# Optimization experiments

Hardware: AMD Instinct MI355X
Metric: run time of the kernel (lower is better)

## Reference

```python
import math
import jax, jax.numpy as jnp
import numpy as np

B, S, D, H = 2, 2048, 1024, 16
DK = D // H


def setup_inputs() -> dict:
    key = jax.random.key(0)
    ks = jax.random.split(key, 11)
    s = 0.02
    return {
        "q": jax.random.normal(ks[0], (B, S, D), jnp.float32),
        "k": jax.random.normal(ks[1], (B, S, D), jnp.float32),
        "v": jax.random.normal(ks[2], (B, S, D), jnp.float32),
        # torch nn.Linear weights are [out_features, in_features]
        "w_q": jax.random.normal(ks[3], (D, D), jnp.float32) * s,
        "b_q": jax.random.normal(ks[4], (D,), jnp.float32) * s,
        "w_k": jax.random.normal(ks[5], (D, D), jnp.float32) * s,
        "b_k": jax.random.normal(ks[6], (D,), jnp.float32) * s,
        "w_v": jax.random.normal(ks[7], (D, D), jnp.float32) * s,
        "b_v": jax.random.normal(ks[8], (D,), jnp.float32) * s,
        "w_o": jax.random.normal(ks[9], (D, D), jnp.float32) * s,
        "b_o": jax.random.normal(ks[10], (D,), jnp.float32) * s,
    }


def _heads(x):
    # [B,S,D] -> [B,H,S,DK]
    return x.reshape(B, -1, H, DK).transpose(0, 2, 1, 3)


def reference(q, k, v, w_q, b_q, w_k, b_k, w_v, b_v, w_o, b_o):
    query = _heads(q @ w_q.T + b_q)
    key = _heads(k @ w_k.T + b_k)
    value = _heads(v @ w_v.T + b_v)
    # scaled scores [B,H,S,S]
    scores = jnp.einsum("bhqd,bhkd->bhqk", query, key) / math.sqrt(DK)
    # NOTE: the original torch code calls scores.softmax(dim=-1) but DISCARDS
    # the result (softmax is not in-place); faithfully, raw scaled scores are
    # used to weight the values. Dropout disabled (p=0 / eval).
    attn_out = jnp.einsum("bhqk,bhkd->bhqd", scores, value)
    x = attn_out.transpose(0, 2, 1, 3).reshape(B, -1, H * DK)
    return x @ w_o.T + b_o
```

## Files before the change

kernel.cpp:

```cpp
#include <hip/hip_runtime.h>
#include <hip/hip_bf16.h>

typedef unsigned short ushort_t;
typedef unsigned int uint32;
typedef __attribute__((ext_vector_type(8))) short short8;
typedef __attribute__((ext_vector_type(4))) float f32x4;

#define NB 2
#define NS 2048
#define ND 1024
#define NH 16

__device__ __forceinline__ float bf2f(ushort_t u) {
  return __uint_as_float(((uint32)u) << 16);
}
__device__ __forceinline__ ushort_t f2bf(float x) {
  uint32 u = __float_as_uint(x);
  uint32 r = u + 0x7FFFu + ((u >> 16) & 1u);
  return (ushort_t)(r >> 16);
}

__device__ __forceinline__ void gload16(const void* g, void* l) {
  __builtin_amdgcn_global_load_lds(
      (const __attribute__((address_space(1))) void*)g,
      (__attribute__((address_space(3))) void*)l, 16, 0, 0);
}

__global__ __launch_bounds__(256) void convert_kernel(
    const float* q, const float* k, const float* v, const float* wq,
    const float* wk, const float* wv, const float* wo, ushort_t* Xq,
    ushort_t* Xk, ushort_t* Xv, ushort_t* Wq, ushort_t* Wk, ushort_t* Wv,
    ushort_t* Wo) {
  const int blk = blockIdx.x;
  const float* src;
  ushort_t* dst;
  int base;
  if (blk < 2048) { src = q; dst = Xq; base = blk; }
  else if (blk < 4096) { src = k; dst = Xk; base = blk - 2048; }
  else if (blk < 6144) { src = v; dst = Xv; base = blk - 4096; }
  else if (blk < 6656) { src = wq; dst = Wq; base = blk - 6144; }
  else if (blk < 7168) { src = wk; dst = Wk; base = blk - 6656; }
  else if (blk < 7680) { src = wv; dst = Wv; base = blk - 7168; }
  else { src = wo; dst = Wo; base = blk - 7680; }
  const size_t off = (size_t)base * 2048 + (size_t)threadIdx.x * 8;
  const float4 v0 = *(const float4*)&src[off];
  const float4 v1 = *(const float4*)&src[off + 4];
  short8 o;
  o[0] = (short)f2bf(v0.x); o[1] = (short)f2bf(v0.y);
  o[2] = (short)f2bf(v0.z); o[3] = (short)f2bf(v0.w);
  o[4] = (short)f2bf(v1.x); o[5] = (short)f2bf(v1.y);
  o[6] = (short)f2bf(v1.z); o[7] = (short)f2bf(v1.w);
  *(short8*)&dst[off] = o;
}

template <typename OutT>
__device__ __forceinline__ void gemm128x128(
    const ushort_t* __restrict__ A, const ushort_t* __restrict__ Bt,
    const float* __restrict__ bias, OutT* __restrict__ Y, int bm, int bn) {
  constexpr int K = 1024;
  constexpr int NY = 1024;
  __shared__ __align__(16) ushort_t sA[128 * 32];
  __shared__ __align__(16) ushort_t sB[128 * 32];
  const int t = threadIdx.x;
  const int lane = t & 63;
  const int w = t >> 6;
  const int wr = w >> 1, wc = w & 1;
  const int r15 = lane & 15, kh = lane >> 4;
  const int m0 = bm * 128, n0 = bn * 128;

  f32x4 acc[4][4] = {};

  const int row0 = t >> 2, cc8 = (t & 3) * 8;
  const ushort_t* gA0 = A + (size_t)(m0 + row0) * K + cc8;
  const ushort_t* gA1 = A + (size_t)(m0 + row0 + 64) * K + cc8;
  const ushort_t* gB0 = Bt + (size_t)(n0 + row0) * K + cc8;
  const ushort_t* gB1 = Bt + (size_t)(n0 + row0 + 64) * K + cc8;
  ushort_t* lA0 = &sA[t * 8];
  ushort_t* lA1 = &sA[(t + 256) * 8];
  ushort_t* lB0 = &sB[t * 8];
  ushort_t* lB1 = &sB[(t + 256) * 8];

  for (int k0 = 0; k0 < K; k0 += 32) {
    gload16(gA0 + k0, lA0);
    gload16(gA1 + k0, lA1);
    gload16(gB0 + k0, lB0);
    gload16(gB1 + k0, lB1);
    __syncthreads();
    short8 af[4], bfr[4];
#pragma unroll
    for (int m = 0; m < 4; ++m)
      af[m] = *(const short8*)&sA[(wr * 64 + m * 16 + r15) * 32 + kh * 8];
#pragma unroll
    for (int n = 0; n < 4; ++n)
      bfr[n] = *(const short8*)&sB[(wc * 64 + n * 16 + r15) * 32 + kh * 8];
#pragma unroll
    for (int m = 0; m < 4; ++m)
#pragma unroll
      for (int n = 0; n < 4; ++n)
        acc[m][n] = __builtin_amdgcn_mfma_f32_16x16x32_bf16(af[m], bfr[n],
                                                            acc[m][n], 0, 0, 0);
    __syncthreads();
  }

  const int orow0 = m0 + wr * 64 + kh * 4;
  const int ocol0 = n0 + wc * 64 + r15;
#pragma unroll
  for (int m = 0; m < 4; ++m) {
#pragma unroll
    for (int n = 0; n < 4; ++n) {
      const int col = ocol0 + n * 16;
      const float bv = bias[col];
#pragma unroll
      for (int j = 0; j < 4; ++j) {
        const int row = orow0 + m * 16 + j;
        const float val = acc[m][n][j] + bv;
        if constexpr (__is_same(OutT, ushort_t))
          Y[(size_t)row * NY + col] = f2bf(val);
        else
          Y[(size_t)row * NY + col] = val;
      }
    }
  }
}

template <typename OutT>
__device__ __forceinline__ void gemm64x128(
    const ushort_t* __restrict__ A, const ushort_t* __restrict__ Bt,
    const float* __restrict__ bias, OutT* __restrict__ Y, int bm, int bn) {
  constexpr int K = 1024;
  constexpr int NY = 1024;
  __shared__ __align__(16) ushort_t sA[64 * 32];
  __shared__ __align__(16) ushort_t sB[128 * 32];
  const int t = threadIdx.x;
  const int lane = t & 63;
  const int w = t >> 6;
  const int wr = w >> 1, wc = w & 1;
  const int r15 = lane & 15, kh = lane >> 4;
  const int m0 = bm * 64, n0 = bn * 128;

  f32x4 acc[2][4] = {};

  const int rowA = t >> 2, cc8 = (t & 3) * 8;
  const ushort_t* gA = A + (size_t)(m0 + rowA) * K + cc8;
  const ushort_t* gB0 = Bt + (size_t)(n0 + rowA) * K + cc8;
  const ushort_t* gB1 = Bt + (size_t)(n0 + rowA + 64) * K + cc8;
  ushort_t* lA = &sA[t * 8];
  ushort_t* lB0 = &sB[t * 8];
  ushort_t* lB1 = &sB[(t + 256) * 8];

  for (int k0 = 0; k0 < K; k0 += 32) {
    gload16(gA + k0, lA);
    gload16(gB0 + k0, lB0);
    gload16(gB1 + k0, lB1);
    __syncthreads();
    short8 af[2], bfr[4];
#pragma unroll
    for (int m = 0; m < 2; ++m)
      af[m] = *(const short8*)&sA[(wr * 32 + m * 16 + r15) * 32 + kh * 8];
#pragma unroll
    for (int n = 0; n < 4; ++n)
      bfr[n] = *(const short8*)&sB[(wc * 64 + n * 16 + r15) * 32 + kh * 8];
#pragma unroll
    for (int m = 0; m < 2; ++m)
#pragma unroll
      for (int n = 0; n < 4; ++n)
        acc[m][n] = __builtin_amdgcn_mfma_f32_16x16x32_bf16(af[m], bfr[n],
                                                            acc[m][n], 0, 0, 0);
    __syncthreads();
  }

  const int orow0 = m0 + wr * 32 + kh * 4;
  const int ocol0 = n0 + wc * 64 + r15;
#pragma unroll
  for (int m = 0; m < 2; ++m) {
#pragma unroll
    for (int n = 0; n < 4; ++n) {
      const int col = ocol0 + n * 16;
      const float bv = bias[col];
#pragma unroll
      for (int j = 0; j < 4; ++j) {
        const int row = orow0 + m * 16 + j;
        const float val = acc[m][n][j] + bv;
        if constexpr (__is_same(OutT, ushort_t))
          Y[(size_t)row * NY + col] = f2bf(val);
        else
          Y[(size_t)row * NY + col] = val;
      }
    }
  }
}

__global__ __launch_bounds__(256) void proj_qkv_kernel(
    const ushort_t* Xq, const ushort_t* Xk, const ushort_t* Xv,
    const ushort_t* Wq, const ushort_t* Wk, const ushort_t* Wv,
    const float* bq, const float* bk, const float* bv,
    ushort_t* Qb, ushort_t* Kb, ushort_t* Vb) {
  const int blk = blockIdx.x;
  const int tsel = blk >> 8;
  int rem = blk & 255;
  rem = (rem & 7) * 32 + (rem >> 3);
  const int bm = rem >> 3, bn = rem & 7;
  const ushort_t* A = tsel == 0 ? Xq : (tsel == 1 ? Xk : Xv);
  const ushort_t* Bt = tsel == 0 ? Wq : (tsel == 1 ? Wk : Wv);
  const float* bias = tsel == 0 ? bq : (tsel == 1 ? bk : bv);
  ushort_t* Y = tsel == 0 ? Qb : (tsel == 1 ? Kb : Vb);
  gemm128x128<ushort_t>(A, Bt, bias, Y, bm, bn);
}

__global__ __launch_bounds__(256) void out_gemm_kernel(
    const ushort_t* Qb, const ushort_t* Ct, const float* bo, float* out) {
  int blk = blockIdx.x;
  blk = (blk & 7) * 64 + (blk >> 3);
  const int bm = blk >> 3, bn = blk & 7;
  const ushort_t* Bt = Ct + (size_t)(bm >> 5) * 1024 * 1024;
  gemm64x128<float>(Qb, Bt, bo, out, bm, bn);
}

__global__ __launch_bounds__(256) void kv_outer_kernel(
    const ushort_t* __restrict__ Kb, const ushort_t* __restrict__ Vb,
    float* __restrict__ Mpart) {
  const int bh = blockIdx.x >> 4;
  const int c = blockIdx.x & 15;
  const int b = bh >> 4, h = bh & 15;
  __shared__ __align__(16) ushort_t sK[128][64];
  __shared__ __align__(16) ushort_t sV[128][64];
  const int t = threadIdx.x;
  const ushort_t* baseK = Kb + (size_t)(b * NS + c * 128) * ND + h * 64;
  const ushort_t* baseV = Vb + (size_t)(b * NS + c * 128) * ND + h * 64;
#pragma unroll
  for (int i = 0; i < 4; ++i) {
    const int ch = t + i * 256;
    const int row = ch >> 3, cc = ch & 7;
    *(short8*)&sK[row][cc * 8] = *(const short8*)&baseK[(size_t)row * ND + cc * 8];
    *(short8*)&sV[row][cc * 8] = *(const short8*)&baseV[(size_t)row * ND + cc * 8];
  }
  __syncthreads();
  const int d1 = (t & 15) * 4, d2 = (t >> 4) * 4;
  float acc[4][4] = {};
  for (int s = 0; s < 128; ++s) {
    const uint2 ku = *(const uint2*)&sK[s][d1];
    const uint2 vu = *(const uint2*)&sV[s][d2];
    float kx[4], vx[4];
    kx[0] = __uint_as_float(ku.x << 16);
    kx[1] = __uint_as_float(ku.x & 0xFFFF0000u);
    kx[2] = __uint_as_float(ku.y << 16);
    kx[3] = __uint_as_float(ku.y & 0xFFFF0000u);
    vx[0] = __uint_as_float(vu.x << 16);
    vx[1] = __uint_as_float(vu.x & 0xFFFF0000u);
    vx[2] = __uint_as_float(vu.y << 16);
    vx[3] = __uint_as_float(vu.y & 0xFFFF0000u);
#pragma unroll
    for (int a2 = 0; a2 < 4; ++a2)
#pragma unroll
      for (int b2 = 0; b2 < 4; ++b2) acc[a2][b2] += kx[a2] * vx[b2];
  }
  float* outp = Mpart + ((size_t)bh * 16 + c) * 4096;
#pragma unroll
  for (int a2 = 0; a2 < 4; ++a2)
#pragma unroll
    for (int b2 = 0; b2 < 4; ++b2)
      outp[(d1 + a2) * 64 + (d2 + b2)] = acc[a2][b2];
}

__global__ __launch_bounds__(256) void reduce_M_kernel(
    const float* __restrict__ Mpart, float* __restrict__ Mred) {
  const int idx = blockIdx.x * 256 + threadIdx.x;
  const int bh = idx >> 12, e = idx & 4095;
  float s = 0.f;
#pragma unroll
  for (int c = 0; c < 16; ++c) s += Mpart[((size_t)bh * 16 + c) * 4096 + e];
  Mred[idx] = s * 0.125f;
}

__global__ __launch_bounds__(256) void build_C_kernel(
    const float* __restrict__ Mred, const ushort_t* __restrict__ Wo,
    ushort_t* __restrict__ Ct) {
  const int blk = blockIdx.x;
  const int b = blk >> 8, h = (blk >> 4) & 15, jb = blk & 15;
  __shared__ float sM[64][65];
  __shared__ __align__(16) ushort_t sW[64][72];
  const int t = threadIdx.x;
  const float* Mp = Mred + (size_t)(b * 16 + h) * 4096;
#pragma unroll
  for (int i = 0; i < 16; ++i) {
    const int e = t + i * 256;
    sM[e >> 6][e & 63] = Mp[e];
  }
  const int j0 = jb * 64;
#pragma unroll
  for (int i = 0; i < 2; ++i) {
    const int ch = t + i * 256;
    const int row = ch >> 3, cc = ch & 7;
    *(short8*)&sW[row][cc * 8] =
        *(const short8*)&Wo[(size_t)(j0 + row) * ND + h * 64 + cc * 8];
  }
  __syncthreads();
  const int kk = (t & 15) * 4, jj = (t >> 4) * 4;
  float acc[4][4] = {};
  for (int i = 0; i < 64; ++i) {
    float mv[4], wv[4];
#pragma unroll
    for (int a2 = 0; a2 < 4; ++a2) mv[a2] = sM[kk + a2][i];
#pragma unroll
    for (int b2 = 0; b2 < 4; ++b2) wv[b2] = bf2f(sW[jj + b2][i]);
#pragma unroll
    for (int a2 = 0; a2 < 4; ++a2)
#pragma unroll
      for (int b2 = 0; b2 < 4; ++b2) acc[a2][b2] += mv[a2] * wv[b2];
  }
#pragma unroll
  for (int a2 = 0; a2 < 4; ++a2)
#pragma unroll
    for (int b2 = 0; b2 < 4; ++b2)
      Ct[((size_t)b * ND + j0 + jj + b2) * ND + h * 64 + kk + a2] =
          f2bf(acc[a2][b2]);
}

extern "C" void kernel_launch(void* const* d_in, const int* in_sizes, int n_in,
                              void* d_out, int out_size, void* d_ws,
                              size_t ws_size, hipStream_t stream) {
  (void)in_sizes; (void)n_in; (void)out_size; (void)ws_size;
  const float* q = (const float*)d_in[0];
  const float* k = (const float*)d_in[1];
  const float* v = (const float*)d_in[2];
  const float* wq = (const float*)d_in[3];
  const float* bq = (const float*)d_in[4];
  const float* wk = (const float*)d_in[5];
  const float* bk = (const float*)d_in[6];
  const float* wv = (const float*)d_in[7];
  const float* bv = (const float*)d_in[8];
  const float* wo = (const float*)d_in[9];
  const float* bo = (const float*)d_in[10];
  float* out = (float*)d_out;

  const size_t MB = 1048576;
  char* ws = (char*)d_ws;
  ushort_t* Xq = (ushort_t*)(ws + 0 * MB);
  ushort_t* Xk = (ushort_t*)(ws + 8 * MB);
  ushort_t* Xv = (ushort_t*)(ws + 16 * MB);
  ushort_t* Wq = (ushort_t*)(ws + 24 * MB);
  ushort_t* Wk = (ushort_t*)(ws + 26 * MB);
  ushort_t* Wv = (ushort_t*)(ws + 28 * MB);
  ushort_t* Wo = (ushort_t*)(ws + 30 * MB);
  ushort_t* Qb = (ushort_t*)(ws + 32 * MB);
  ushort_t* Kb = (ushort_t*)(ws + 40 * MB);
  ushort_t* Vb = (ushort_t*)(ws + 48 * MB);
  float* Mpart = (float*)(ws + 0 * MB);
  float* Mred = (float*)(ws + 8 * MB);
  ushort_t* Ct = (ushort_t*)(ws + 8 * MB + 524288);

  hipLaunchKernelGGL(convert_kernel, dim3(8192), dim3(256), 0, stream, q, k, v,
                     wq, wk, wv, wo, Xq, Xk, Xv, Wq, Wk, Wv, Wo);
  hipLaunchKernelGGL(proj_qkv_kernel, dim3(768), dim3(256), 0, stream, Xq, Xk,
                     Xv, Wq, Wk, Wv, bq, bk, bv, Qb, Kb, Vb);
  hipLaunchKernelGGL(kv_outer_kernel, dim3(512), dim3(256), 0, stream, Kb, Vb,
                     Mpart);
  hipLaunchKernelGGL(reduce_M_kernel, dim3(512), dim3(256), 0, stream, Mpart,
                     Mred);
  hipLaunchKernelGGL(build_C_kernel, dim3(512), dim3(256), 0, stream, Mred, Wo,
                     Ct);
  hipLaunchKernelGGL(out_gemm_kernel, dim3(512), dim3(256), 0, stream, Qb, Ct,
                     bo, out);
}
```

Before: 205.9 us.

## Fuse fp32-to-bf16 activation conversion into QKV GEMM and double-buffer GEMMs

Removes the separate conversion pass over the q/k/v activations. The QKV projection GEMM now loads fp32 A tiles into registers, converts them to bf16 and writes them to LDS itself, so the bf16 activation copies are no longer written to and read back from global memory. Both the projection GEMM and the output GEMM gain double-buffered LDS with prefetch of the next tile, which lets loads overlap MFMA work. The cost is doubled LDS per block, more registers, and fp32 activation reads: each A tile is re-read by all 8 column blocks at twice the byte size.

```diff
diff --git a/kernel.cpp b/kernel.cpp
--- a/kernel.cpp
+++ b/kernel.cpp
@@ -4,6 +4,7 @@
 typedef unsigned short ushort_t;
 typedef unsigned int uint32;
 typedef __attribute__((ext_vector_type(8))) short short8;
+typedef __attribute__((ext_vector_type(4))) short short4_t;
 typedef __attribute__((ext_vector_type(4))) float f32x4;
 
 #define NB 2
@@ -26,22 +27,17 @@
       (__attribute__((address_space(3))) void*)l, 16, 0, 0);
 }
 
-__global__ __launch_bounds__(256) void convert_kernel(
-    const float* q, const float* k, const float* v, const float* wq,
-    const float* wk, const float* wv, const float* wo, ushort_t* Xq,
-    ushort_t* Xk, ushort_t* Xv, ushort_t* Wq, ushort_t* Wk, ushort_t* Wv,
-    ushort_t* Wo) {
+__global__ __launch_bounds__(256) void convert_w_kernel(
+    const float* wq, const float* wk, const float* wv, const float* wo,
+    ushort_t* Wq, ushort_t* Wk, ushort_t* Wv, ushort_t* Wo) {
   const int blk = blockIdx.x;
   const float* src;
   ushort_t* dst;
   int base;
-  if (blk < 2048) { src = q; dst = Xq; base = blk; }
-  else if (blk < 4096) { src = k; dst = Xk; base = blk - 2048; }
-  else if (blk < 6144) { src = v; dst = Xv; base = blk - 4096; }
-  else if (blk < 6656) { src = wq; dst = Wq; base = blk - 6144; }
-  else if (blk < 7168) { src = wk; dst = Wk; base = blk - 6656; }
-  else if (blk < 7680) { src = wv; dst = Wv; base = blk - 7168; }
-  else { src = wo; dst = Wo; base = blk - 7680; }
+  if (blk < 512) { src = wq; dst = Wq; base = blk; }
+  else if (blk < 1024) { src = wk; dst = Wk; base = blk - 512; }
+  else if (blk < 1536) { src = wv; dst = Wv; base = blk - 1024; }
+  else { src = wo; dst = Wo; base = blk - 1536; }
   const size_t off = (size_t)base * 2048 + (size_t)threadIdx.x * 8;
   const float4 v0 = *(const float4*)&src[off];
   const float4 v1 = *(const float4*)&src[off + 4];
@@ -53,14 +49,14 @@
   *(short8*)&dst[off] = o;
 }
 
-template <typename OutT>
-__device__ __forceinline__ void gemm128x128(
-    const ushort_t* __restrict__ A, const ushort_t* __restrict__ Bt,
-    const float* __restrict__ bias, OutT* __restrict__ Y, int bm, int bn) {
+__device__ __forceinline__ void gemm128x128_f32A(
+    const float* __restrict__ A, const ushort_t* __restrict__ Bt,
+    const float* __restrict__ bias, ushort_t* __restrict__ Y, int bm, int bn) {
   constexpr int K = 1024;
+  constexpr int NT = K / 32;
   constexpr int NY = 1024;
-  __shared__ __align__(16) ushort_t sA[128 * 32];
-  __shared__ __align__(16) ushort_t sB[128 * 32];
+  __shared__ __align__(16) ushort_t sA[2 * 128 * 32];
+  __shared__ __align__(16) ushort_t sB[2 * 128 * 32];
   const int t = threadIdx.x;
   const int lane = t & 63;
   const int w = t >> 6;
@@ -70,29 +66,60 @@
 
   f32x4 acc[4][4] = {};
 
-  const int row0 = t >> 2, cc8 = (t & 3) * 8;
-  const ushort_t* gA0 = A + (size_t)(m0 + row0) * K + cc8;
-  const ushort_t* gA1 = A + (size_t)(m0 + row0 + 64) * K + cc8;
-  const ushort_t* gB0 = Bt + (size_t)(n0 + row0) * K + cc8;
-  const ushort_t* gB1 = Bt + (size_t)(n0 + row0 + 64) * K + cc8;
-  ushort_t* lA0 = &sA[t * 8];
-  ushort_t* lA1 = &sA[(t + 256) * 8];
-  ushort_t* lB0 = &sB[t * 8];
-  ushort_t* lB1 = &sB[(t + 256) * 8];
-
-  for (int k0 = 0; k0 < K; k0 += 32) {
-    gload16(gA0 + k0, lA0);
-    gload16(gA1 + k0, lA1);
-    gload16(gB0 + k0, lB0);
-    gload16(gB1 + k0, lB1);
-    __syncthreads();
+  const int rowA = t >> 3, c4 = t & 7;
+  const float* gA = A + (size_t)(m0 + rowA) * K + c4 * 4;
+  const int rowB = t >> 2, cc8 = (t & 3) * 8;
+  const ushort_t* gB0 = Bt + (size_t)(n0 + rowB) * K + cc8;
+  const ushort_t* gB1 = Bt + (size_t)(n0 + rowB + 64) * K + cc8;
+
+  float4 ar[4];
+#define LOADA(tile)                                                        \
+  {                                                                        \
+    const int k0_ = (tile) * 32;                                           \
+    _Pragma("unroll") for (int i = 0; i < 4; ++i) ar[i] =                  \
+        *(const float4*)&gA[(size_t)(i * 32) * K + k0_];                   \
+  }
+#define WRITEA(bufsel)                                                     \
+  {                                                                        \
+    ushort_t* sAw_ = &sA[(bufsel) * 4096];                                 \
+    _Pragma("unroll") for (int i = 0; i < 4; ++i) {                        \
+      short4_t s_;                                                         \
+      s_[0] = (short)f2bf(ar[i].x);                                        \
+      s_[1] = (short)f2bf(ar[i].y);                                        \
+      s_[2] = (short)f2bf(ar[i].z);                                        \
+      s_[3] = (short)f2bf(ar[i].w);                                        \
+      *(short4_t*)&sAw_[(rowA + i * 32) * 32 + c4 * 4] = s_;               \
+    }                                                                      \
+  }
+#define STAGEB(tile, bufsel)                                               \
+  {                                                                        \
+    ushort_t* sBw_ = &sB[(bufsel) * 4096];                                 \
+    gload16(gB0 + (tile) * 32, &sBw_[t * 8]);                              \
+    gload16(gB1 + (tile) * 32, &sBw_[(t + 256) * 8]);                      \
+  }
+
+  LOADA(0);
+  STAGEB(0, 0);
+  WRITEA(0);
+  LOADA(1);
+  __syncthreads();
+
+  int cur = 0;
+  for (int tt = 0; tt < NT; ++tt) {
+    if (tt + 1 < NT) {
+      WRITEA(cur ^ 1);
+      STAGEB(tt + 1, cur ^ 1);
+      if (tt + 2 < NT) LOADA(tt + 2);
+    }
+    const ushort_t* sAc = &sA[cur * 4096];
+    const ushort_t* sBc = &sB[cur * 4096];
     short8 af[4], bfr[4];
 #pragma unroll
     for (int m = 0; m < 4; ++m)
-      af[m] = *(const short8*)&sA[(wr * 64 + m * 16 + r15) * 32 + kh * 8];
+      af[m] = *(const short8*)&sAc[(wr * 64 + m * 16 + r15) * 32 + kh * 8];
 #pragma unroll
     for (int n = 0; n < 4; ++n)
-      bfr[n] = *(const short8*)&sB[(wc * 64 + n * 16 + r15) * 32 + kh * 8];
+      bfr[n] = *(const short8*)&sBc[(wc * 64 + n * 16 + r15) * 32 + kh * 8];
 #pragma unroll
     for (int m = 0; m < 4; ++m)
 #pragma unroll
@@ -100,7 +127,11 @@
         acc[m][n] = __builtin_amdgcn_mfma_f32_16x16x32_bf16(af[m], bfr[n],
                                                             acc[m][n], 0, 0, 0);
     __syncthreads();
-  }
+    cur ^= 1;
+  }
+#undef LOADA
+#undef WRITEA
+#undef STAGEB
 
   const int orow0 = m0 + wr * 64 + kh * 4;
   const int ocol0 = n0 + wc * 64 + r15;
@@ -113,24 +144,20 @@
 #pragma unroll
       for (int j = 0; j < 4; ++j) {
         const int row = orow0 + m * 16 + j;
-        const float val = acc[m][n][j] + bv;
-        if constexpr (__is_same(OutT, ushort_t))
-          Y[(size_t)row * NY + col] = f2bf(val);
-        else
-          Y[(size_t)row * NY + col] = val;
+        Y[(size_t)row * NY + col] = f2bf(acc[m][n][j] + bv);
       }
     }
   }
 }
 
-template <typename OutT>
-__device__ __forceinline__ void gemm64x128(
+__device__ __forceinline__ void gemm64x128_dbuf(
     const ushort_t* __restrict__ A, const ushort_t* __restrict__ Bt,
-    const float* __restrict__ bias, OutT* __restrict__ Y, int bm, int bn) {
+    const float* __restrict__ bias, float* __restrict__ Y, int bm, int bn) {
   constexpr int K = 1024;
+  constexpr int NT = K / 32;
   constexpr int NY = 1024;
-  __shared__ __align__(16) ushort_t sA[64 * 32];
-  __shared__ __align__(16) ushort_t sB[128 * 32];
+  __shared__ __align__(16) ushort_t sA[2 * 64 * 32];
+  __shared__ __align__(16) ushort_t sB[2 * 128 * 32];
   const int t = threadIdx.x;
   const int lane = t & 63;
   const int w = t >> 6;
@@ -140,26 +167,34 @@
 
   f32x4 acc[2][4] = {};
 
-  const int rowA = t >> 2, cc8 = (t & 3) * 8;
-  const ushort_t* gA = A + (size_t)(m0 + rowA) * K + cc8;
-  const ushort_t* gB0 = Bt + (size_t)(n0 + rowA) * K + cc8;
-  const ushort_t* gB1 = Bt + (size_t)(n0 + rowA + 64) * K + cc8;
-  ushort_t* lA = &sA[t * 8];
-  ushort_t* lB0 = &sB[t * 8];
-  ushort_t* lB1 = &sB[(t + 256) * 8];
-
-  for (int k0 = 0; k0 < K; k0 += 32) {
-    gload16(gA + k0, lA);
-    gload16(gB0 + k0, lB0);
-    gload16(gB1 + k0, lB1);
-    __syncthreads();
+  const int rowX = t >> 2, cc8 = (t & 3) * 8;
+  const ushort_t* gA = A + (size_t)(m0 + rowX) * K + cc8;
+  const ushort_t* gB0 = Bt + (size_t)(n0 + rowX) * K + cc8;
+  const ushort_t* gB1 = Bt + (size_t)(n0 + rowX + 64) * K + cc8;
+
+#define STAGE(tile, bufsel)                                                \
+  {                                                                        \
+    const int k0_ = (tile) * 32;                                           \
+    gload16(gA + k0_, &sA[(bufsel) * 2048 + t * 8]);                       \
+    gload16(gB0 + k0_, &sB[(bufsel) * 4096 + t * 8]);                      \
+    gload16(gB1 + k0_, &sB[(bufsel) * 4096 + (t + 256) * 8]);              \
+  }
+
+  STAGE(0, 0);
+  __syncthreads();
+
+  int cur = 0;
+  for (int tt = 0; tt < NT; ++tt) {
+    if (tt + 1 < NT) STAGE(tt + 1, cur ^ 1);
+    const ushort_t* sAc = &sA[cur * 2048];
+    const ushort_t* sBc = &sB[cur * 4096];
     short8 af[2], bfr[4];
 #pragma unroll
     for (int m = 0; m < 2; ++m)
-      af[m] = *(const short8*)&sA[(wr * 32 + m * 16 + r15) * 32 + kh * 8];
+      af[m] = *(const short8*)&sAc[(wr * 32 + m * 16 + r15) * 32 + kh * 8];
 #pragma unroll
     for (int n = 0; n < 4; ++n)
-      bfr[n] = *(const short8*)&sB[(wc * 64 + n * 16 + r15) * 32 + kh * 8];
+      bfr[n] = *(const short8*)&sBc[(wc * 64 + n * 16 + r15) * 32 + kh * 8];
 #pragma unroll
     for (int m = 0; m < 2; ++m)
 #pragma unroll
@@ -167,7 +202,9 @@
         acc[m][n] = __builtin_amdgcn_mfma_f32_16x16x32_bf16(af[m], bfr[n],
                                                             acc[m][n], 0, 0, 0);
     __syncthreads();
-  }
+    cur ^= 1;
+  }
+#undef STAGE
 
   const int orow0 = m0 + wr * 32 + kh * 4;
   const int ocol0 = n0 + wc * 64 + r15;
@@ -180,18 +217,14 @@
 #pragma unroll
       for (int j = 0; j < 4; ++j) {
         const int row = orow0 + m * 16 + j;
-        const float val = acc[m][n][j] + bv;
-        if constexpr (__is_same(OutT, ushort_t))
-          Y[(size_t)row * NY + col] = f2bf(val);
-        else
-          Y[(size_t)row * NY + col] = val;
+        Y[(size_t)row * NY + col] = acc[m][n][j] + bv;
       }
     }
   }
 }
 
 __global__ __launch_bounds__(256) void proj_qkv_kernel(
-    const ushort_t* Xq, const ushort_t* Xk, const ushort_t* Xv,
+    const float* q, const float* k, const float* v,
     const ushort_t* Wq, const ushort_t* Wk, const ushort_t* Wv,
     const float* bq, const float* bk, const float* bv,
     ushort_t* Qb, ushort_t* Kb, ushort_t* Vb) {
@@ -200,11 +233,11 @@
   int rem = blk & 255;
   rem = (rem & 7) * 32 + (rem >> 3);
   const int bm = rem >> 3, bn = rem & 7;
-  const ushort_t* A = tsel == 0 ? Xq : (tsel == 1 ? Xk : Xv);
+  const float* A = tsel == 0 ? q : (tsel == 1 ? k : v);
   const ushort_t* Bt = tsel == 0 ? Wq : (tsel == 1 ? Wk : Wv);
   const float* bias = tsel == 0 ? bq : (tsel == 1 ? bk : bv);
   ushort_t* Y = tsel == 0 ? Qb : (tsel == 1 ? Kb : Vb);
-  gemm128x128<ushort_t>(A, Bt, bias, Y, bm, bn);
+  gemm128x128_f32A(A, Bt, bias, Y, bm, bn);
 }
 
 __global__ __launch_bounds__(256) void out_gemm_kernel(
@@ -213,7 +246,7 @@
   blk = (blk & 7) * 64 + (blk >> 3);
   const int bm = blk >> 3, bn = blk & 7;
   const ushort_t* Bt = Ct + (size_t)(bm >> 5) * 1024 * 1024;
-  gemm64x128<float>(Qb, Bt, bo, out, bm, bn);
+  gemm64x128_dbuf(Qb, Bt, bo, out, bm, bn);
 }
 
 __global__ __launch_bounds__(256) void kv_outer_kernel(
@@ -335,24 +368,21 @@
 
   const size_t MB = 1048576;
   char* ws = (char*)d_ws;
-  ushort_t* Xq = (ushort_t*)(ws + 0 * MB);
-  ushort_t* Xk = (ushort_t*)(ws + 8 * MB);
-  ushort_t* Xv = (ushort_t*)(ws + 16 * MB);
-  ushort_t* Wq = (ushort_t*)(ws + 24 * MB);
-  ushort_t* Wk = (ushort_t*)(ws + 26 * MB);
-  ushort_t* Wv = (ushort_t*)(ws + 28 * MB);
-  ushort_t* Wo = (ushort_t*)(ws + 30 * MB);
-  ushort_t* Qb = (ushort_t*)(ws + 32 * MB);
-  ushort_t* Kb = (ushort_t*)(ws + 40 * MB);
-  ushort_t* Vb = (ushort_t*)(ws + 48 * MB);
-  float* Mpart = (float*)(ws + 0 * MB);
-  float* Mred = (float*)(ws + 8 * MB);
-  ushort_t* Ct = (ushort_t*)(ws + 8 * MB + 524288);
-
-  hipLaunchKernelGGL(convert_kernel, dim3(8192), dim3(256), 0, stream, q, k, v,
-                     wq, wk, wv, wo, Xq, Xk, Xv, Wq, Wk, Wv, Wo);
-  hipLaunchKernelGGL(proj_qkv_kernel, dim3(768), dim3(256), 0, stream, Xq, Xk,
-                     Xv, Wq, Wk, Wv, bq, bk, bv, Qb, Kb, Vb);
+  ushort_t* Wq = (ushort_t*)(ws + 0 * MB);
+  ushort_t* Wk = (ushort_t*)(ws + 2 * MB);
+  ushort_t* Wv = (ushort_t*)(ws + 4 * MB);
+  ushort_t* Wo = (ushort_t*)(ws + 6 * MB);
+  ushort_t* Qb = (ushort_t*)(ws + 8 * MB);
+  ushort_t* Kb = (ushort_t*)(ws + 16 * MB);
+  ushort_t* Vb = (ushort_t*)(ws + 24 * MB);
+  float* Mpart = (float*)(ws + 32 * MB);
+  float* Mred = (float*)(ws + 40 * MB);
+  ushort_t* Ct = (ushort_t*)(ws + 40 * MB + 524288);
+
+  hipLaunchKernelGGL(convert_w_kernel, dim3(2048), dim3(256), 0, stream, wq, wk,
+                     wv, wo, Wq, Wk, Wv, Wo);
+  hipLaunchKernelGGL(proj_qkv_kernel, dim3(768), dim3(256), 0, stream, q, k, v,
+                     Wq, Wk, Wv, bq, bk, bv, Qb, Kb, Vb);
   hipLaunchKernelGGL(kv_outer_kernel, dim3(512), dim3(256), 0, stream, Kb, Vb,
                      Mpart);
   hipLaunchKernelGGL(reduce_M_kernel, dim3(512), dim3(256), 0, stream, Mpart,
```

New measurement: 209.9 us. No clear change (+2.0%).

## Fold Q projection into the output matrix to skip the Q GEMM

Applied to the files above, without the earlier changes.

Instead of projecting Q (a 4096x1024x1024 GEMM) and then multiplying by the per-batch combined matrix Ct, this precomputes E = Ct·Wq per batch (a smaller 1024^3 GEMM per batch) plus a folded bias Ct·bq+bo. The final GEMM then consumes the converted raw q directly. It adds a transpose kernel for Wq, a small GEMV kernel for the bias and an extra GEMM launch. The extra bf16 rounding of E is a precision risk, and the 16-block bias kernel may serialize.

```diff
diff --git a/kernel.cpp b/kernel.cpp
--- a/kernel.cpp
+++ b/kernel.cpp
@@ -27,10 +27,9 @@
 }
 
 __global__ __launch_bounds__(256) void convert_kernel(
-    const float* q, const float* k, const float* v, const float* wq,
-    const float* wk, const float* wv, const float* wo, ushort_t* Xq,
-    ushort_t* Xk, ushort_t* Xv, ushort_t* Wq, ushort_t* Wk, ushort_t* Wv,
-    ushort_t* Wo) {
+    const float* q, const float* k, const float* v, const float* wk,
+    const float* wv, const float* wo, ushort_t* Xq, ushort_t* Xk, ushort_t* Xv,
+    ushort_t* Wk, ushort_t* Wv, ushort_t* Wo) {
   const int blk = blockIdx.x;
   const float* src;
   ushort_t* dst;
@@ -38,10 +37,9 @@
   if (blk < 2048) { src = q; dst = Xq; base = blk; }
   else if (blk < 4096) { src = k; dst = Xk; base = blk - 2048; }
   else if (blk < 6144) { src = v; dst = Xv; base = blk - 4096; }
-  else if (blk < 6656) { src = wq; dst = Wq; base = blk - 6144; }
-  else if (blk < 7168) { src = wk; dst = Wk; base = blk - 6656; }
-  else if (blk < 7680) { src = wv; dst = Wv; base = blk - 7168; }
-  else { src = wo; dst = Wo; base = blk - 7680; }
+  else if (blk < 6656) { src = wk; dst = Wk; base = blk - 6144; }
+  else if (blk < 7168) { src = wv; dst = Wv; base = blk - 6656; }
+  else { src = wo; dst = Wo; base = blk - 7168; }
   const size_t off = (size_t)base * 2048 + (size_t)threadIdx.x * 8;
   const float4 v0 = *(const float4*)&src[off];
   const float4 v1 = *(const float4*)&src[off + 4];
@@ -51,6 +49,36 @@
   o[4] = (short)f2bf(v1.x); o[5] = (short)f2bf(v1.y);
   o[6] = (short)f2bf(v1.z); o[7] = (short)f2bf(v1.w);
   *(short8*)&dst[off] = o;
+}
+
+__global__ __launch_bounds__(256) void transp_wq_kernel(const float* wq,
+                                                        ushort_t* WqT) {
+  const int tk = blockIdx.x >> 4, td = blockIdx.x & 15;
+  __shared__ float sT[64][65];
+  const int t = threadIdx.x;
+  const int r = t >> 2;
+  const int cbase = (t & 3) * 16;
+  const float* src = wq + (size_t)(tk * 64 + r) * ND + td * 64 + cbase;
+#pragma unroll
+  for (int i = 0; i < 4; ++i) {
+    const float4 v4 = *(const float4*)&src[i * 4];
+    sT[cbase + i * 4 + 0][r] = v4.x;
+    sT[cbase + i * 4 + 1][r] = v4.y;
+    sT[cbase + i * 4 + 2][r] = v4.z;
+    sT[cbase + i * 4 + 3][r] = v4.w;
+  }
+  __syncthreads();
+  const int dl = t >> 2;
+  const int kc = (t & 3) * 16;
+  ushort_t* dst = WqT + (size_t)(td * 64 + dl) * ND + tk * 64 + kc;
+  short8 o0, o1;
+#pragma unroll
+  for (int e = 0; e < 8; ++e) {
+    o0[e] = (short)f2bf(sT[dl][kc + e]);
+    o1[e] = (short)f2bf(sT[dl][kc + 8 + e]);
+  }
+  *(short8*)&dst[0] = o0;
+  *(short8*)&dst[8] = o1;
 }
 
 template <typename OutT>
@@ -109,7 +137,7 @@
 #pragma unroll
     for (int n = 0; n < 4; ++n) {
       const int col = ocol0 + n * 16;
-      const float bv = bias[col];
+      const float bv = bias ? bias[col] : 0.0f;
 #pragma unroll
       for (int j = 0; j < 4; ++j) {
         const int row = orow0 + m * 16 + j;
@@ -176,7 +204,7 @@
 #pragma unroll
     for (int n = 0; n < 4; ++n) {
       const int col = ocol0 + n * 16;
-      const float bv = bias[col];
+      const float bv = bias ? bias[col] : 0.0f;
 #pragma unroll
       for (int j = 0; j < 4; ++j) {
         const int row = orow0 + m * 16 + j;
@@ -190,30 +218,45 @@
   }
 }
 
-__global__ __launch_bounds__(256) void proj_qkv_kernel(
-    const ushort_t* Xq, const ushort_t* Xk, const ushort_t* Xv,
-    const ushort_t* Wq, const ushort_t* Wk, const ushort_t* Wv,
-    const float* bq, const float* bk, const float* bv,
-    ushort_t* Qb, ushort_t* Kb, ushort_t* Vb) {
+__global__ __launch_bounds__(256) void proj_kv_kernel(
+    const ushort_t* Xk, const ushort_t* Xv, const ushort_t* Wk,
+    const ushort_t* Wv, const float* bk, const float* bv, ushort_t* Kb,
+    ushort_t* Vb) {
   const int blk = blockIdx.x;
   const int tsel = blk >> 8;
   int rem = blk & 255;
   rem = (rem & 7) * 32 + (rem >> 3);
   const int bm = rem >> 3, bn = rem & 7;
-  const ushort_t* A = tsel == 0 ? Xq : (tsel == 1 ? Xk : Xv);
-  const ushort_t* Bt = tsel == 0 ? Wq : (tsel == 1 ? Wk : Wv);
-  const float* bias = tsel == 0 ? bq : (tsel == 1 ? bk : bv);
-  ushort_t* Y = tsel == 0 ? Qb : (tsel == 1 ? Kb : Vb);
+  const ushort_t* A = tsel == 0 ? Xk : Xv;
+  const ushort_t* Bt = tsel == 0 ? Wk : Wv;
+  const float* bias = tsel == 0 ? bk : bv;
+  ushort_t* Y = tsel == 0 ? Kb : Vb;
   gemm128x128<ushort_t>(A, Bt, bias, Y, bm, bn);
 }
 
-__global__ __launch_bounds__(256) void out_gemm_kernel(
-    const ushort_t* Qb, const ushort_t* Ct, const float* bo, float* out) {
+__global__ __launch_bounds__(256) void e_gemm_kernel(const ushort_t* Ct,
+                                                     const ushort_t* WqT,
+                                                     ushort_t* E) {
+  int blk = blockIdx.x;
+  blk = (blk & 7) * 32 + (blk >> 3);
+  const int b = blk >> 7;
+  const int rem = blk & 127;
+  const int bm = rem >> 3, bn = rem & 7;
+  const ushort_t* A = Ct + (size_t)b * ND * ND;
+  ushort_t* Y = E + (size_t)b * ND * ND;
+  gemm64x128<ushort_t>(A, WqT, nullptr, Y, bm, bn);
+}
+
+__global__ __launch_bounds__(256) void out_gemm_kernel(const ushort_t* Xq,
+                                                       const ushort_t* E,
+                                                       const float* fbias,
+                                                       float* out) {
   int blk = blockIdx.x;
   blk = (blk & 7) * 64 + (blk >> 3);
   const int bm = blk >> 3, bn = blk & 7;
-  const ushort_t* Bt = Ct + (size_t)(bm >> 5) * 1024 * 1024;
-  gemm64x128<float>(Qb, Bt, bo, out, bm, bn);
+  const int batch = bm >> 5;
+  const ushort_t* Bt = E + (size_t)batch * ND * ND;
+  gemm64x128<float>(Xq, Bt, fbias + batch * ND, out, bm, bn);
 }
 
 __global__ __launch_bounds__(256) void kv_outer_kernel(
@@ -314,6 +357,27 @@
     for (int b2 = 0; b2 < 4; ++b2)
       Ct[((size_t)b * ND + j0 + jj + b2) * ND + h * 64 + kk + a2] =
           f2bf(acc[a2][b2]);
+}
+
+__global__ __launch_bounds__(256) void f_kernel(const ushort_t* __restrict__ Ct,
+                                                const float* __restrict__ bq,
+                                                const float* __restrict__ bo,
+                                                float* __restrict__ fbias) {
+  const int b = blockIdx.x >> 3;
+  const int j = (blockIdx.x & 7) * 128 + (threadIdx.x >> 1);
+  const int half = threadIdx.x & 1;
+  const ushort_t* row = Ct + ((size_t)b * ND + j) * ND + half * 512;
+  const float* bqh = bq + half * 512;
+  float s = 0.f;
+  for (int c = 0; c < 64; ++c) {
+    const short8 v8 = *(const short8*)&row[c * 8];
+#pragma unroll
+    for (int e = 0; e < 8; ++e) s += bf2f((ushort_t)v8[e]) * bqh[c * 8 + e];
+  }
+  __shared__ float red[256];
+  red[threadIdx.x] = s;
+  __syncthreads();
+  if (half == 0) fbias[b * ND + j] = red[threadIdx.x] + red[threadIdx.x + 1] + bo[j];
 }
 
 extern "C" void kernel_launch(void* const* d_in, const int* in_sizes, int n_in,
@@ -338,27 +402,34 @@
   ushort_t* Xq = (ushort_t*)(ws + 0 * MB);
   ushort_t* Xk = (ushort_t*)(ws + 8 * MB);
   ushort_t* Xv = (ushort_t*)(ws + 16 * MB);
-  ushort_t* Wq = (ushort_t*)(ws + 24 * MB);
-  ushort_t* Wk = (ushort_t*)(ws + 26 * MB);
-  ushort_t* Wv = (ushort_t*)(ws + 28 * MB);
-  ushort_t* Wo = (ushort_t*)(ws + 30 * MB);
-  ushort_t* Qb = (ushort_t*)(ws + 32 * MB);
-  ushort_t* Kb = (ushort_t*)(ws + 40 * MB);
-  ushort_t* Vb = (ushort_t*)(ws + 48 * MB);
-  float* Mpart = (float*)(ws + 0 * MB);
-  float* Mred = (float*)(ws + 8 * MB);
-  ushort_t* Ct = (ushort_t*)(ws + 8 * MB + 524288);
-
-  hipLaunchKernelGGL(convert_kernel, dim3(8192), dim3(256), 0, stream, q, k, v,
-                     wq, wk, wv, wo, Xq, Xk, Xv, Wq, Wk, Wv, Wo);
-  hipLaunchKernelGGL(proj_qkv_kernel, dim3(768), dim3(256), 0, stream, Xq, Xk,
-                     Xv, Wq, Wk, Wv, bq, bk, bv, Qb, Kb, Vb);
+  ushort_t* Wk = (ushort_t*)(ws + 24 * MB);
+  ushort_t* Wv = (ushort_t*)(ws + 26 * MB);
+  ushort_t* Wo = (ushort_t*)(ws + 28 * MB);
+  ushort_t* WqT = (ushort_t*)(ws + 30 * MB);
+  ushort_t* Kb = (ushort_t*)(ws + 32 * MB);
+  ushort_t* Vb = (ushort_t*)(ws + 40 * MB);
+  float* Mpart = (float*)(ws + 8 * MB);
+  float* Mred = (float*)(ws + 16 * MB);
+  ushort_t* Ct = (ushort_t*)(ws + 16 * MB + 524288);
+  float* fbias = (float*)(ws + 16 * MB + 524288 + 4 * MB);
+  ushort_t* E = (ushort_t*)(ws + 24 * MB);
+
+  hipLaunchKernelGGL(convert_kernel, dim3(7680), dim3(256), 0, stream, q, k, v,
+                     wk, wv, wo, Xq, Xk, Xv, Wk, Wv, Wo);
+  hipLaunchKernelGGL(transp_wq_kernel, dim3(256), dim3(256), 0, stream, wq,
+                     WqT);
+  hipLaunchKernelGGL(proj_kv_kernel, dim3(512), dim3(256), 0, stream, Xk, Xv,
+                     Wk, Wv, bk, bv, Kb, Vb);
   hipLaunchKernelGGL(kv_outer_kernel, dim3(512), dim3(256), 0, stream, Kb, Vb,
                      Mpart);
   hipLaunchKernelGGL(reduce_M_kernel, dim3(512), dim3(256), 0, stream, Mpart,
                      Mred);
   hipLaunchKernelGGL(build_C_kernel, dim3(512), dim3(256), 0, stream, Mred, Wo,
                      Ct);
-  hipLaunchKernelGGL(out_gemm_kernel, dim3(512), dim3(256), 0, stream, Qb, Ct,
-                     bo, out);
-}
+  hipLaunchKernelGGL(f_kernel, dim3(16), dim3(256), 0, stream, Ct, bq, bo,
+                     fbias);
+  hipLaunchKernelGGL(e_gemm_kernel, dim3(256), dim3(256), 0, stream, Ct, WqT,
+                     E);
+  hipLaunchKernelGGL(out_gemm_kernel, dim3(512), dim3(256), 0, stream, Xq, E,
+                     fbias, out);
+}
```

Result: slower. 229.1 us (+11.3%).

## Use BK=64 XOR-swizzled GEMM tiles and fold M reduction into atomics

Applied to the files above, without the earlier changes.

Both bf16 GEMMs now stage 64-wide K slices per iteration, using an XOR-swizzled LDS layout to avoid bank conflicts. This halves the number of barrier pairs per K loop. The separate reduce kernel is removed: partial KᵀV outer products are atomically added into a buffer zeroed by extra convert blocks, and the 1/8 scale moves into build_C. This saves one launch and the partial-buffer traffic, at the cost of float atomic contention and non-deterministic summation order.

```diff
diff --git a/kernel.cpp b/kernel.cpp
--- a/kernel.cpp
+++ b/kernel.cpp
@@ -30,8 +30,15 @@
     const float* q, const float* k, const float* v, const float* wq,
     const float* wk, const float* wv, const float* wo, ushort_t* Xq,
     ushort_t* Xk, ushort_t* Xv, ushort_t* Wq, ushort_t* Wk, ushort_t* Wv,
-    ushort_t* Wo) {
+    ushort_t* Wo, float* Mred) {
   const int blk = blockIdx.x;
+  if (blk >= 8192) {
+    const size_t o = (size_t)(blk - 8192) * 2048 + (size_t)threadIdx.x * 8;
+    const float4 z = make_float4(0.f, 0.f, 0.f, 0.f);
+    *(float4*)&Mred[o] = z;
+    *(float4*)&Mred[o + 4] = z;
+    return;
+  }
   const float* src;
   ushort_t* dst;
   int base;
@@ -54,13 +61,13 @@
 }
 
 template <typename OutT>
-__device__ __forceinline__ void gemm128x128(
+__device__ __forceinline__ void gemm128x128_bk64(
     const ushort_t* __restrict__ A, const ushort_t* __restrict__ Bt,
     const float* __restrict__ bias, OutT* __restrict__ Y, int bm, int bn) {
   constexpr int K = 1024;
   constexpr int NY = 1024;
-  __shared__ __align__(16) ushort_t sA[128 * 32];
-  __shared__ __align__(16) ushort_t sB[128 * 32];
+  __shared__ __align__(16) ushort_t sA[128 * 64];
+  __shared__ __align__(16) ushort_t sB[128 * 64];
   const int t = threadIdx.x;
   const int lane = t & 63;
   const int w = t >> 6;
@@ -70,35 +77,39 @@
 
   f32x4 acc[4][4] = {};
 
-  const int row0 = t >> 2, cc8 = (t & 3) * 8;
-  const ushort_t* gA0 = A + (size_t)(m0 + row0) * K + cc8;
-  const ushort_t* gA1 = A + (size_t)(m0 + row0 + 64) * K + cc8;
-  const ushort_t* gB0 = Bt + (size_t)(n0 + row0) * K + cc8;
-  const ushort_t* gB1 = Bt + (size_t)(n0 + row0 + 64) * K + cc8;
-  ushort_t* lA0 = &sA[t * 8];
-  ushort_t* lA1 = &sA[(t + 256) * 8];
-  ushort_t* lB0 = &sB[t * 8];
-  ushort_t* lB1 = &sB[(t + 256) * 8];
-
-  for (int k0 = 0; k0 < K; k0 += 32) {
-    gload16(gA0 + k0, lA0);
-    gload16(gA1 + k0, lA1);
-    gload16(gB0 + k0, lB0);
-    gload16(gB1 + k0, lB1);
+  const int rowS = t >> 3;
+  const int srcSlot = (t & 7) ^ (rowS & 7);
+  const ushort_t* gA = A + (size_t)(m0 + rowS) * K + srcSlot * 8;
+  const ushort_t* gB = Bt + (size_t)(n0 + rowS) * K + srcSlot * 8;
+
+  for (int k0 = 0; k0 < K; k0 += 64) {
+#pragma unroll
+    for (int i = 0; i < 4; ++i) {
+      gload16(gA + (size_t)(i * 32) * K + k0, &sA[(t + i * 256) * 8]);
+      gload16(gB + (size_t)(i * 32) * K + k0, &sB[(t + i * 256) * 8]);
+    }
     __syncthreads();
-    short8 af[4], bfr[4];
-#pragma unroll
-    for (int m = 0; m < 4; ++m)
-      af[m] = *(const short8*)&sA[(wr * 64 + m * 16 + r15) * 32 + kh * 8];
-#pragma unroll
-    for (int n = 0; n < 4; ++n)
-      bfr[n] = *(const short8*)&sB[(wc * 64 + n * 16 + r15) * 32 + kh * 8];
-#pragma unroll
-    for (int m = 0; m < 4; ++m)
-#pragma unroll
-      for (int n = 0; n < 4; ++n)
-        acc[m][n] = __builtin_amdgcn_mfma_f32_16x16x32_bf16(af[m], bfr[n],
-                                                            acc[m][n], 0, 0, 0);
+#pragma unroll
+    for (int kk = 0; kk < 2; ++kk) {
+      const int slotbase = kk * 4 + kh;
+      short8 af[4], bfr[4];
+#pragma unroll
+      for (int m = 0; m < 4; ++m) {
+        const int row = wr * 64 + m * 16 + r15;
+        af[m] = *(const short8*)&sA[row * 64 + ((slotbase ^ (row & 7)) * 8)];
+      }
+#pragma unroll
+      for (int n = 0; n < 4; ++n) {
+        const int row = wc * 64 + n * 16 + r15;
+        bfr[n] = *(const short8*)&sB[row * 64 + ((slotbase ^ (row & 7)) * 8)];
+      }
+#pragma unroll
+      for (int m = 0; m < 4; ++m)
+#pragma unroll
+        for (int n = 0; n < 4; ++n)
+          acc[m][n] = __builtin_amdgcn_mfma_f32_16x16x32_bf16(
+              af[m], bfr[n], acc[m][n], 0, 0, 0);
+    }
     __syncthreads();
   }
 
@@ -124,13 +135,13 @@
 }
 
 template <typename OutT>
-__device__ __forceinline__ void gemm64x128(
+__device__ __forceinline__ void gemm64x128_bk64(
     const ushort_t* __restrict__ A, const ushort_t* __restrict__ Bt,
     const float* __restrict__ bias, OutT* __restrict__ Y, int bm, int bn) {
   constexpr int K = 1024;
   constexpr int NY = 1024;
-  __shared__ __align__(16) ushort_t sA[64 * 32];
-  __shared__ __align__(16) ushort_t sB[128 * 32];
+  __shared__ __align__(16) ushort_t sA[64 * 64];
+  __shared__ __align__(16) ushort_t sB[128 * 64];
   const int t = threadIdx.x;
   const int lane = t & 63;
   const int w = t >> 6;
@@ -140,32 +151,40 @@
 
   f32x4 acc[2][4] = {};
 
-  const int rowA = t >> 2, cc8 = (t & 3) * 8;
-  const ushort_t* gA = A + (size_t)(m0 + rowA) * K + cc8;
-  const ushort_t* gB0 = Bt + (size_t)(n0 + rowA) * K + cc8;
-  const ushort_t* gB1 = Bt + (size_t)(n0 + rowA + 64) * K + cc8;
-  ushort_t* lA = &sA[t * 8];
-  ushort_t* lB0 = &sB[t * 8];
-  ushort_t* lB1 = &sB[(t + 256) * 8];
-
-  for (int k0 = 0; k0 < K; k0 += 32) {
-    gload16(gA + k0, lA);
-    gload16(gB0 + k0, lB0);
-    gload16(gB1 + k0, lB1);
+  const int rowS = t >> 3;
+  const int srcSlot = (t & 7) ^ (rowS & 7);
+  const ushort_t* gA = A + (size_t)(m0 + rowS) * K + srcSlot * 8;
+  const ushort_t* gB = Bt + (size_t)(n0 + rowS) * K + srcSlot * 8;
+
+  for (int k0 = 0; k0 < K; k0 += 64) {
+#pragma unroll
+    for (int i = 0; i < 2; ++i)
+      gload16(gA + (size_t)(i * 32) * K + k0, &sA[(t + i * 256) * 8]);
+#pragma unroll
+    for (int i = 0; i < 4; ++i)
+      gload16(gB + (size_t)(i * 32) * K + k0, &sB[(t + i * 256) * 8]);
     __syncthreads();
-    short8 af[2], bfr[4];
-#pragma unroll
-    for (int m = 0; m < 2; ++m)
-      af[m] = *(const short8*)&sA[(wr * 32 + m * 16 + r15) * 32 + kh * 8];
-#pragma unroll
-    for (int n = 0; n < 4; ++n)
-      bfr[n] = *(const short8*)&sB[(wc * 64 + n * 16 + r15) * 32 + kh * 8];
-#pragma unroll
-    for (int m = 0; m < 2; ++m)
-#pragma unroll
-      for (int n = 0; n < 4; ++n)
-        acc[m][n] = __builtin_amdgcn_mfma_f32_16x16x32_bf16(af[m], bfr[n],
-                                                            acc[m][n], 0, 0, 0);
+#pragma unroll
+    for (int kk = 0; kk < 2; ++kk) {
+      const int slotbase = kk * 4 + kh;
+      short8 af[2], bfr[4];
+#pragma unroll
+      for (int m = 0; m < 2; ++m) {
+        const int row = wr * 32 + m * 16 + r15;
+        af[m] = *(const short8*)&sA[row * 64 + ((slotbase ^ (row & 7)) * 8)];
+      }
+#pragma unroll
+      for (int n = 0; n < 4; ++n) {
+        const int row = wc * 64 + n * 16 + r15;
+        bfr[n] = *(const short8*)&sB[row * 64 + ((slotbase ^ (row & 7)) * 8)];
+      }
+#pragma unroll
+      for (int m = 0; m < 2; ++m)
+#pragma unroll
+        for (int n = 0; n < 4; ++n)
+          acc[m][n] = __builtin_amdgcn_mfma_f32_16x16x32_bf16(
+              af[m], bfr[n], acc[m][n], 0, 0, 0);
+    }
     __syncthreads();
   }
 
@@ -204,7 +223,7 @@
   const ushort_t* Bt = tsel == 0 ? Wq : (tsel == 1 ? Wk : Wv);
   const float* bias = tsel == 0 ? bq : (tsel == 1 ? bk : bv);
   ushort_t* Y = tsel == 0 ? Qb : (tsel == 1 ? Kb : Vb);
-  gemm128x128<ushort_t>(A, Bt, bias, Y, bm, bn);
+  gemm128x128_bk64<ushort_t>(A, Bt, bias, Y, bm, bn);
 }
 
 __global__ __launch_bounds__(256) void out_gemm_kernel(
@@ -213,12 +232,12 @@
   blk = (blk & 7) * 64 + (blk >> 3);
   const int bm = blk >> 3, bn = blk & 7;
   const ushort_t* Bt = Ct + (size_t)(bm >> 5) * 1024 * 1024;
-  gemm64x128<float>(Qb, Bt, bo, out, bm, bn);
+  gemm64x128_bk64<float>(Qb, Bt, bo, out, bm, bn);
 }
 
 __global__ __launch_bounds__(256) void kv_outer_kernel(
     const ushort_t* __restrict__ Kb, const ushort_t* __restrict__ Vb,
-    float* __restrict__ Mpart) {
+    float* __restrict__ Mred) {
   const int bh = blockIdx.x >> 4;
   const int c = blockIdx.x & 15;
   const int b = bh >> 4, h = bh & 15;
@@ -254,22 +273,12 @@
 #pragma unroll
       for (int b2 = 0; b2 < 4; ++b2) acc[a2][b2] += kx[a2] * vx[b2];
   }
-  float* outp = Mpart + ((size_t)bh * 16 + c) * 4096;
+  float* outp = Mred + (size_t)bh * 4096;
 #pragma unroll
   for (int a2 = 0; a2 < 4; ++a2)
 #pragma unroll
     for (int b2 = 0; b2 < 4; ++b2)
-      outp[(d1 + a2) * 64 + (d2 + b2)] = acc[a2][b2];
-}
-
-__global__ __launch_bounds__(256) void reduce_M_kernel(
-    const float* __restrict__ Mpart, float* __restrict__ Mred) {
-  const int idx = blockIdx.x * 256 + threadIdx.x;
-  const int bh = idx >> 12, e = idx & 4095;
-  float s = 0.f;
-#pragma unroll
-  for (int c = 0; c < 16; ++c) s += Mpart[((size_t)bh * 16 + c) * 4096 + e];
-  Mred[idx] = s * 0.125f;
+      atomicAdd(&outp[(d1 + a2) * 64 + (d2 + b2)], acc[a2][b2]);
 }
 
 __global__ __launch_bounds__(256) void build_C_kernel(
@@ -313,7 +322,7 @@
 #pragma unroll
     for (int b2 = 0; b2 < 4; ++b2)
       Ct[((size_t)b * ND + j0 + jj + b2) * ND + h * 64 + kk + a2] =
-          f2bf(acc[a2][b2]);
+          f2bf(acc[a2][b2] * 0.125f);
 }
 
 extern "C" void kernel_launch(void* const* d_in, const int* in_sizes, int n_in,
@@ -345,17 +354,14 @@
   ushort_t* Qb = (ushort_t*)(ws + 32 * MB);
   ushort_t* Kb = (ushort_t*)(ws + 40 * MB);
   ushort_t* Vb = (ushort_t*)(ws + 48 * MB);
-  float* Mpart = (float*)(ws + 0 * MB);
-  float* Mred = (float*)(ws + 8 * MB);
-  ushort_t* Ct = (ushort_t*)(ws + 8 * MB + 524288);
-
-  hipLaunchKernelGGL(convert_kernel, dim3(8192), dim3(256), 0, stream, q, k, v,
-                     wq, wk, wv, wo, Xq, Xk, Xv, Wq, Wk, Wv, Wo);
+  float* Mred = (float*)(ws + 56 * MB);
+  ushort_t* Ct = (ushort_t*)(ws + 57 * MB);
+
+  hipLaunchKernelGGL(convert_kernel, dim3(8256), dim3(256), 0, stream, q, k, v,
+                     wq, wk, wv, wo, Xq, Xk, Xv, Wq, Wk, Wv, Wo, Mred);
   hipLaunchKernelGGL(proj_qkv_kernel, dim3(768), dim3(256), 0, stream, Xq, Xk,
                      Xv, Wq, Wk, Wv, bq, bk, bv, Qb, Kb, Vb);
   hipLaunchKernelGGL(kv_outer_kernel, dim3(512), dim3(256), 0, stream, Kb, Vb,
-                     Mpart);
-  hipLaunchKernelGGL(reduce_M_kernel, dim3(512), dim3(256), 0, stream, Mpart,
                      Mred);
   hipLaunchKernelGGL(build_C_kernel, dim3(512), dim3(256), 0, stream, Mred, Wo,
                      Ct);
```

After: 211.0 us. +2.5%, slower.
